# Performance work log

Measured on AMD Instinct MI355X. Metric: run time of the kernel, lower is better.

Reference implementation:

```python
import jax, jax.numpy as jnp
import numpy as np

NUM_BEAMS = 4
EOS = 2
PAD = 0
T = 16  # max_tokens decode steps
NEG = jnp.float32(-1e32)


def setup_inputs() -> dict:
    key = jax.random.key(0)
    ks = jax.random.split(key, 12)
    Vv, E, D, L, bs = 32000, 512, 512, 2, 16
    s = 0.05
    n = lambda k, sh: (jax.random.normal(k, sh, dtype=jnp.float32) * s)
    return {
        'inputs': jax.random.randint(ks[0], (1, bs), 0, Vv),
        'h0': n(ks[1], (L, bs, D)),
        'c0': n(ks[2], (L, bs, D)),
        'emb': n(ks[3], (Vv, E)),
        'Wih0': n(ks[4], (4 * D, E)),
        'Whh0': n(ks[5], (4 * D, D)),
        'b0': n(ks[6], (4 * D,)),
        'Wih1': n(ks[7], (4 * D, D)),
        'Whh1': n(ks[8], (4 * D, D)),
        'b1': n(ks[9], (4 * D,)),
        'Wp': n(ks[10], (D, Vv)),
        'bp': n(ks[11], (Vv,)),
    }


def _lstm(x, h, c, Wih, Whh, b):
    z = x @ Wih.T + h @ Whh.T + b
    i, f, g, o = jnp.split(z, 4, axis=-1)
    c = jax.nn.sigmoid(f) * c + jax.nn.sigmoid(i) * jnp.tanh(g)
    h = jax.nn.sigmoid(o) * jnp.tanh(c)
    return h, c


def reference(inputs, h0, c0, emb, Wih0, Whh0, b0, Wih1, Whh1, b1, Wp, bp):
    bs = inputs.shape[1]
    nb = NUM_BEAMS
    B = bs * nb
    Vv = emb.shape[0]

    def cell(tok, h, c):
        # one decode step of the 2-layer LSTM + projection; tok: (B,)
        x = emb[tok]
        h0n, c0n = _lstm(x, h[0], c[0], Wih0, Whh0, b0)
        h1n, c1n = _lstm(h0n, h[1], c[1], Wih1, Whh1, b1)
        logits = h1n @ Wp + bp  # (B, V)
        return logits, jnp.stack([h0n, h1n]), jnp.stack([c0n, c1n])

    offs = jnp.arange(bs)[:, None] * nb  # batch-major beam layout b*nb+beam

    # ---- iteration 0: all beams identical, keep beam 0 only ----
    tokens = jnp.repeat(inputs[0], nb)           # (B,)
    h = jnp.repeat(h0, nb, axis=1)               # (L, B, D)
    c = jnp.repeat(c0, nb, axis=1)
    logits0, h, c = cell(tokens, h, c)
    lp0 = jax.nn.log_softmax(logits0, axis=-1).reshape(bs, nb, Vv)[:, 0, :]
    logprobs, beams = jax.lax.top_k(lp0, nb)     # (bs, nb)
    pidx = (beams // Vv + offs).reshape(-1)      # parents == 0
    tokens = (beams % Vv).reshape(-1)
    h = h[:, pidx]
    c = c[:, pidx]
    finished = tokens == EOS
    beam_out = jnp.zeros((T + 1, B), dtype=tokens.dtype)
    beam_out = beam_out.at[0].set(jnp.repeat(inputs[0], nb)[pidx]).at[1].set(tokens)

    # ---- iterations 1..T-1 ----
    def step(carry, t):
        tokens, h, c, logprobs, finished, beam_out = carry
        logits, h, c = cell(tokens, h, c)
        new_lp = jax.nn.log_softmax(logits, axis=-1).reshape(bs, nb, Vv) + logprobs[:, :, None]
        # finished beams: forced to emit PAD with unchanged cumulative logprob
        masked = jnp.full((bs, nb, Vv), NEG).at[:, :, PAD].set(logprobs)
        fin = finished.reshape(bs, nb)
        new_lp = jnp.where(fin[:, :, None], masked, new_lp)
        logprobs, beams = jax.lax.top_k(new_lp.reshape(bs, nb * Vv), nb)
        pidx = (beams // Vv + offs).reshape(-1)
        toks = (beams % Vv).reshape(-1)
        h = h[:, pidx]
        c = c[:, pidx]
        finished = finished[pidx] | (toks == EOS)
        beam_out = beam_out[:, pidx].at[t + 1].set(toks)
        return (toks, h, c, logprobs, finished, beam_out), logits

    carry0 = (tokens, h, c, logprobs, finished, beam_out)
    carry_f, logits_seq = jax.lax.scan(step, carry0, jnp.arange(1, T))
    logits_all = jnp.concatenate([logits0[None], logits_seq], axis=0)  # (T, B, V)
    beam_outputs = carry_f[5].reshape(T + 1, bs, nb)
    return logits_all, beam_outputs
```

## Files before the change

### kernel.cpp

```cpp
#include <hip/hip_runtime.h>
#include <math.h>

#define BS     16
#define NB     4
#define BB     64
#define DD     512
#define VV     32000
#define TSTEPS 16
#define EOSTOK 2
#define NEGF   (-1e32f)
#define VT     64
#define NVT    (VV / VT)

__device__ __forceinline__ bool better(float av, int ai, float bv, int bi_) {
    return (av > bv) || (av == bv && ai < bi_);
}

__device__ __forceinline__ void glds4(const float* src, float* dst) {
    __builtin_amdgcn_global_load_lds((const __attribute__((address_space(1))) void*)src,
                                     (__attribute__((address_space(3))) void*)dst, 4, 0, 0);
}
__device__ __forceinline__ void glds16(const float* src, float* dst) {
    __builtin_amdgcn_global_load_lds((const __attribute__((address_space(1))) void*)src,
                                     (__attribute__((address_space(3))) void*)dst, 16, 0, 0);
}

__global__ void init_kernel(const int* __restrict__ inputs,
                            const float* __restrict__ h0, const float* __restrict__ c0,
                            float* __restrict__ h0s, float* __restrict__ c0s,
                            float* __restrict__ h1s, float* __restrict__ c1s,
                            int* __restrict__ tokens, int* __restrict__ pidx,
                            int* __restrict__ fin, float* __restrict__ lp,
                            int* __restrict__ bo)
{
    int tid = blockIdx.x * blockDim.x + threadIdx.x;
    int total = BB * DD;
    for (int i = tid; i < total; i += gridDim.x * blockDim.x) {
        int b = i / DD;
        int d = i % DD;
        int src0 = 0 * BS * DD + (b >> 2) * DD + d;
        int src1 = 1 * BS * DD + (b >> 2) * DD + d;
        h0s[i] = h0[src0];
        c0s[i] = c0[src0];
        h1s[i] = h0[src1];
        c1s[i] = c0[src1];
    }
    if (tid < BB) {
        tokens[tid] = inputs[tid >> 2];
        pidx[tid]   = tid;
        fin[tid]    = 0;
        lp[tid]     = 0.0f;
        bo[0 * BB + tid] = inputs[tid >> 2];
        for (int r = 1; r <= TSTEPS; r++) bo[r * BB + tid] = 0;
    }
}

__global__ __launch_bounds__(256) void lstm_kernel(
    const float* __restrict__ xbase, const int* __restrict__ xrow,
    const float* __restrict__ hsrc,  const float* __restrict__ csrc,
    const int* __restrict__ prow,
    float* __restrict__ hdst, float* __restrict__ cdst,
    const float* __restrict__ Wih, const float* __restrict__ Whh,
    const float* __restrict__ bias)
{
    __shared__ float U[64][129];
    __shared__ float Wl[4][1024];
    __shared__ double Z[4][64];
    __shared__ int rows_s[64], prows_s[64];
    int tid = threadIdx.x;
    int j = blockIdx.x;
    int b = tid & 63;
    int g = tid >> 6;
    int lane = tid & 63;
    int w = tid >> 6;

    #pragma unroll
    for (int i = 0; i < 4; i++) {
        int s0 = i * 256 + w * 64;
        int gg = s0 >> 8;
        int hh = (s0 >> 7) & 1;
        int c0 = s0 & 127;
        const float* rowbase = (hh ? Whh : Wih) + (size_t)(gg * DD + j) * DD;
        glds16(rowbase + 4 * (c0 + lane), (float*)Wl + 4 * s0);
    }
    if (tid < 64) {
        rows_s[tid]  = xrow ? xrow[tid] : tid;
        prows_s[tid] = prow[tid];
    }

    double a0 = 0.0, a1 = 0.0, a2 = 0.0, a3 = 0.0;
    for (int ch = 0; ch < 8; ch++) {
        int k0 = ch * 128;
        __syncthreads();
        #pragma unroll
        for (int i = 0; i < 32; i++) {
            int e0 = i * 256 + w * 64;
            int bb = e0 >> 7;
            int kk0 = e0 & 127;
            const float* src;
            if (k0 < 512) src = xbase + (size_t)rows_s[bb] * DD + k0 + kk0 + lane;
            else          src = hsrc + (size_t)prows_s[bb] * DD + (k0 - 512) + kk0 + lane;
            glds4(src, &U[bb][kk0]);
        }
        __syncthreads();
        const float* Wrow = &Wl[g][k0];
        #pragma unroll 8
        for (int kk = 0; kk < 128; kk += 4) {
            a0 = fma((double)U[b][kk + 0], (double)Wrow[kk + 0], a0);
            a1 = fma((double)U[b][kk + 1], (double)Wrow[kk + 1], a1);
            a2 = fma((double)U[b][kk + 2], (double)Wrow[kk + 2], a2);
            a3 = fma((double)U[b][kk + 3], (double)Wrow[kk + 3], a3);
        }
    }
    Z[g][b] = ((a0 + a1) + (a2 + a3));
    __syncthreads();

    if (tid < 64) {
        double zi = Z[0][b] + (double)bias[0 * DD + j];
        double zf = Z[1][b] + (double)bias[1 * DD + j];
        double zg = Z[2][b] + (double)bias[2 * DD + j];
        double zo = Z[3][b] + (double)bias[3 * DD + j];
        double si = 1.0 / (1.0 + exp(-zi));
        double sf = 1.0 / (1.0 + exp(-zf));
        double so = 1.0 / (1.0 + exp(-zo));
        double cold = (double)csrc[(size_t)prows_s[b] * DD + j];
        double cn = sf * cold + si * tanh(zg);
        double hn = so * tanh(cn);
        hdst[b * DD + j] = (float)hn;
        cdst[b * DD + j] = (float)cn;
    }
}

__global__ __launch_bounds__(256) void proj_kernel(
    const float* __restrict__ h1, const float* __restrict__ Wp,
    const float* __restrict__ bp, float* __restrict__ outf)
{
    __shared__ float sh[64][68];
    __shared__ float sw[64][68];
    int vbase = blockIdx.x * VT;
    int tid = threadIdx.x;
    int lane = tid & 63;
    int w = tid >> 6;
    int b0 = (tid >> 4) * 4;
    int v0 = (tid & 15) * 4;

    double acc[4][4];
    #pragma unroll
    for (int i = 0; i < 4; i++)
        #pragma unroll
        for (int q = 0; q < 4; q++) acc[i][q] = 0.0;

    for (int ch = 0; ch < 8; ch++) {
        int k0 = ch * 64;
        __syncthreads();
        #pragma unroll
        for (int i = 0; i < 16; i++) {
            int bb = i * 4 + w;
            glds4(h1 + (size_t)bb * DD + k0 + lane, &sh[bb][0]);
        }
        #pragma unroll
        for (int i = 0; i < 16; i++) {
            int kk = i * 4 + w;
            glds4(Wp + (size_t)(k0 + kk) * VV + vbase + lane, &sw[kk][0]);
        }
        __syncthreads();
        #pragma unroll
        for (int k4 = 0; k4 < 16; k4++) {
            int k = k4 * 4;
            float4 h4[4], w4[4];
            #pragma unroll
            for (int i = 0; i < 4; i++) h4[i] = *(const float4*)&sh[b0 + i][k];
            #pragma unroll
            for (int kk = 0; kk < 4; kk++) w4[kk] = *(const float4*)&sw[k + kk][v0];
            #pragma unroll
            for (int i = 0; i < 4; i++) {
                const float hh[4] = {h4[i].x, h4[i].y, h4[i].z, h4[i].w};
                #pragma unroll
                for (int kk = 0; kk < 4; kk++) {
                    double hd = (double)hh[kk];
                    const float ww[4] = {w4[kk].x, w4[kk].y, w4[kk].z, w4[kk].w};
                    #pragma unroll
                    for (int q = 0; q < 4; q++)
                        acc[i][q] = fma(hd, (double)ww[q], acc[i][q]);
                }
            }
        }
    }

    #pragma unroll
    for (int i = 0; i < 4; i++) {
        int brow = b0 + i;
        #pragma unroll
        for (int q = 0; q < 4; q++) {
            int v = vbase + v0 + q;
            outf[(size_t)brow * VV + v] = (float)(acc[i][q] + (double)bp[v]);
        }
    }
}

#define NPT 32
__global__ __launch_bounds__(1024) void row_kernel(
    const float* __restrict__ outf, const float* __restrict__ lp,
    const int* __restrict__ fin,
    float* __restrict__ rcv, int* __restrict__ rci, int step0)
{
    int row = blockIdx.x;
    int j   = row & 3;
    int tid = threadIdx.x;
    int base_idx = j * VV;

    float lp_r = step0 ? 0.0f : lp[row];
    int   f    = step0 ? 0    : fin[row];
    if (step0 && j != 0) {
        if (tid < 4) { rcv[row * 4 + tid] = NEGF; rci[row * 4 + tid] = base_idx + tid; }
        return;
    }
    if (f) {
        if (tid < 4) {
            rcv[row * 4 + tid] = (tid == 0) ? lp_r : NEGF;
            rci[row * 4 + tid] = base_idx + tid;
        }
        return;
    }

    const float* xo = outf + (size_t)row * VV;
    __shared__ double red[1024];

    float zreg[NPT];
    double m = -1e300;
    #pragma unroll
    for (int q = 0; q < NPT; q++) {
        int i = tid + q * 1024;
        float zf = 0.0f;
        if (i < VV) {
            zf = xo[i];
            m = fmax(m, (double)zf);
        }
        zreg[q] = zf;
    }

    red[tid] = m; __syncthreads();
    for (int s = 512; s > 0; s >>= 1) {
        if (tid < s) red[tid] = fmax(red[tid], red[tid + s]);
        __syncthreads();
    }
    m = red[0];
    __syncthreads();

    double sum = 0.0;
    #pragma unroll
    for (int q = 0; q < NPT; q++) {
        int i = tid + q * 1024;
        if (i < VV) sum += exp((double)zreg[q] - m);
    }
    red[tid] = sum; __syncthreads();
    for (int s = 512; s > 0; s >>= 1) {
        if (tid < s) red[tid] += red[tid + s];
        __syncthreads();
    }
    double lse = m + log(red[0]);
    __syncthreads();

    float bv[4]; int bx[4];
    #pragma unroll
    for (int q = 0; q < 4; q++) { bv[q] = -3.4e38f; bx[q] = 0x7fffffff; }
    #pragma unroll
    for (int q = 0; q < NPT; q++) {
        int i = tid + q * 1024;
        if (i < VV) {
            float lgp32 = (float)((double)zreg[q] - lse);
            float val   = (float)((double)lp_r + (double)lgp32);
            int idx = base_idx + i;
            if (better(val, idx, bv[3], bx[3])) {
                bv[3] = val; bx[3] = idx;
                #pragma unroll
                for (int s = 3; s > 0; s--) {
                    if (better(bv[s], bx[s], bv[s - 1], bx[s - 1])) {
                        float tv2 = bv[s]; bv[s] = bv[s - 1]; bv[s - 1] = tv2;
                        int ti2 = bx[s]; bx[s] = bx[s - 1]; bx[s - 1] = ti2;
                    }
                }
            }
        }
    }

    __shared__ float sv[1024][4];
    __shared__ int   si_[1024][4];
    #pragma unroll
    for (int q = 0; q < 4; q++) { sv[tid][q] = bv[q]; si_[tid][q] = bx[q]; }
    __syncthreads();
    for (int s = 512; s > 0; s >>= 1) {
        if (tid < s) {
            float av[4], ov[4], mv[4]; int ai[4], oi[4], mi[4];
            #pragma unroll
            for (int q = 0; q < 4; q++) {
                av[q] = sv[tid][q];     ai[q] = si_[tid][q];
                ov[q] = sv[tid + s][q]; oi[q] = si_[tid + s][q];
            }
            int pa = 0, pb = 0;
            #pragma unroll
            for (int q = 0; q < 4; q++) {
                bool takeA = (pb >= 4) || (pa < 4 && better(av[pa], ai[pa], ov[pb], oi[pb]));
                if (takeA) { mv[q] = av[pa]; mi[q] = ai[pa]; pa++; }
                else       { mv[q] = ov[pb]; mi[q] = oi[pb]; pb++; }
            }
            #pragma unroll
            for (int q = 0; q < 4; q++) { sv[tid][q] = mv[q]; si_[tid][q] = mi[q]; }
        }
        __syncthreads();
    }
    if (tid < 4) {
        rcv[row * 4 + tid] = sv[0][tid];
        rci[row * 4 + tid] = si_[0][tid];
    }
}

__global__ void merge_update_kernel(
    const float* __restrict__ rcv, const int* __restrict__ rci,
    float* __restrict__ lp, int* __restrict__ fin,
    int* __restrict__ tokens, int* __restrict__ pidx,
    int* __restrict__ bo, int t)
{
    int b = threadIdx.x;
    int bi = b >> 2, r = b & 3;

    float cv[16]; int ci[16];
    #pragma unroll
    for (int c = 0; c < 16; c++) { cv[c] = rcv[bi * 16 + c]; ci[c] = rci[bi * 16 + c]; }

    int sel = 0;
    #pragma unroll
    for (int c = 0; c < 16; c++) {
        int rank = 0;
        #pragma unroll
        for (int d = 0; d < 16; d++)
            if (d != c && better(cv[d], ci[d], cv[c], ci[c])) rank++;
        if (rank == r) sel = c;
    }

    float v = cv[sel];
    int flat = ci[sel];
    int q = flat / VV;
    int p = q + bi * 4;
    int tok = flat - q * VV;
    int oldfin = fin[p];
    int col[TSTEPS + 1];
    #pragma unroll
    for (int rr = 0; rr <= TSTEPS; rr++) col[rr] = bo[rr * BB + p];
    __syncthreads();
    #pragma unroll
    for (int rr = 0; rr <= TSTEPS; rr++) bo[rr * BB + b] = col[rr];
    bo[(t + 1) * BB + b] = tok;
    fin[b]    = oldfin | (tok == EOSTOK);
    lp[b]     = v;
    tokens[b] = tok;
    pidx[b]   = p;
}

__global__ void final_kernel(const int* __restrict__ bo, float* __restrict__ out)
{
    int i = blockIdx.x * blockDim.x + threadIdx.x;
    if (i < (TSTEPS + 1) * BB) out[i] = (float)bo[i];
}

extern "C" void kernel_launch(void* const* d_in, const int* in_sizes, int n_in,
                              void* d_out, int out_size, void* d_ws, size_t ws_size,
                              hipStream_t stream)
{
    const int*   inputs = (const int*)d_in[0];
    const float* h0   = (const float*)d_in[1];
    const float* c0   = (const float*)d_in[2];
    const float* emb  = (const float*)d_in[3];
    const float* Wih0 = (const float*)d_in[4];
    const float* Whh0 = (const float*)d_in[5];
    const float* b0   = (const float*)d_in[6];
    const float* Wih1 = (const float*)d_in[7];
    const float* Whh1 = (const float*)d_in[8];
    const float* b1   = (const float*)d_in[9];
    const float* Wp   = (const float*)d_in[10];
    const float* bp   = (const float*)d_in[11];
    float* out = (float*)d_out;

    char* w = (char*)d_ws;
    size_t off = 0;
    auto alloc = [&](size_t bytes) { void* p = w + off; off += (bytes + 255) & ~255ULL; return p; };
    float* h0s[2], *c0s[2], *h1s[2], *c1s[2];
    for (int s = 0; s < 2; s++) {
        h0s[s] = (float*)alloc(BB * DD * 4);
        c0s[s] = (float*)alloc(BB * DD * 4);
        h1s[s] = (float*)alloc(BB * DD * 4);
        c1s[s] = (float*)alloc(BB * DD * 4);
    }
    float* rcv   = (float*)alloc(BB * 4 * 4);
    int*   rci   = (int*)alloc(BB * 4 * 4);
    float* lp    = (float*)alloc(BB * 4);
    int* pidx    = (int*)alloc(BB * 4);
    int* tokens  = (int*)alloc(BB * 4);
    int* fin     = (int*)alloc(BB * 4);
    int* bo      = (int*)alloc((TSTEPS + 1) * BB * 4);

    init_kernel<<<128, 256, 0, stream>>>(inputs, h0, c0,
                                         h0s[0], c0s[0], h1s[0], c1s[0],
                                         tokens, pidx, fin, lp, bo);

    for (int t = 0; t < TSTEPS; t++) {
        int s = t & 1, d2 = s ^ 1;
        lstm_kernel<<<512, 256, 0, stream>>>(emb, tokens, h0s[s], c0s[s], pidx,
                                             h0s[d2], c0s[d2], Wih0, Whh0, b0);
        lstm_kernel<<<512, 256, 0, stream>>>(h0s[d2], nullptr, h1s[s], c1s[s], pidx,
                                             h1s[d2], c1s[d2], Wih1, Whh1, b1);

        float* outf = out + (size_t)t * BB * VV;
        proj_kernel<<<NVT, 256, 0, stream>>>(h1s[d2], Wp, bp, outf);
        row_kernel<<<BB, 1024, 0, stream>>>(outf, lp, fin, rcv, rci, t == 0 ? 1 : 0);
        merge_update_kernel<<<1, 64, 0, stream>>>(rcv, rci, lp, fin, tokens, pidx, bo, t);
    }
    final_kernel<<<5, 256, 0, stream>>>(bo, out + (size_t)TSTEPS * BB * VV);
}
```

Measured before the change: 2.851 ms.

## Double-buffer LDS staging in LSTM and projection kernels

New measurement: 2.916 ms. 1.02x slower.

```diff
diff --git a/kernel.cpp b/kernel.cpp
--- a/kernel.cpp
+++ b/kernel.cpp
@@ -63,7 +63,7 @@
     const float* __restrict__ Wih, const float* __restrict__ Whh,
     const float* __restrict__ bias)
 {
-    __shared__ float U[64][129];
+    __shared__ float U[2][64][65];
     __shared__ float Wl[4][1024];
     __shared__ double Z[4][64];
     __shared__ int rows_s[64], prows_s[64];
@@ -87,30 +87,36 @@
         rows_s[tid]  = xrow ? xrow[tid] : tid;
         prows_s[tid] = prow[tid];
     }
+    __syncthreads();
+
+    auto stage = [&](int ch, int buf) {
+        int k0 = ch * 64;
+        #pragma unroll
+        for (int i = 0; i < 16; i++) {
+            int bb = i * 4 + w;
+            const float* src;
+            if (k0 < 512) src = xbase + (size_t)rows_s[bb] * DD + k0 + lane;
+            else          src = hsrc + (size_t)prows_s[bb] * DD + (k0 - 512) + lane;
+            glds4(src, &U[buf][bb][0]);
+        }
+    };
+
+    stage(0, 0);
+    __syncthreads();
 
     double a0 = 0.0, a1 = 0.0, a2 = 0.0, a3 = 0.0;
-    for (int ch = 0; ch < 8; ch++) {
-        int k0 = ch * 128;
+    for (int ch = 0; ch < 16; ch++) {
+        int cur = ch & 1;
+        if (ch < 15) stage(ch + 1, cur ^ 1);
+        const float* Wrow = &Wl[g][ch * 64];
+        #pragma unroll 8
+        for (int kk = 0; kk < 64; kk += 4) {
+            a0 = fma((double)U[cur][b][kk + 0], (double)Wrow[kk + 0], a0);
+            a1 = fma((double)U[cur][b][kk + 1], (double)Wrow[kk + 1], a1);
+            a2 = fma((double)U[cur][b][kk + 2], (double)Wrow[kk + 2], a2);
+            a3 = fma((double)U[cur][b][kk + 3], (double)Wrow[kk + 3], a3);
+        }
         __syncthreads();
-        #pragma unroll
-        for (int i = 0; i < 32; i++) {
-            int e0 = i * 256 + w * 64;
-            int bb = e0 >> 7;
-            int kk0 = e0 & 127;
-            const float* src;
-            if (k0 < 512) src = xbase + (size_t)rows_s[bb] * DD + k0 + kk0 + lane;
-            else          src = hsrc + (size_t)prows_s[bb] * DD + (k0 - 512) + kk0 + lane;
-            glds4(src, &U[bb][kk0]);
-        }
-        __syncthreads();
-        const float* Wrow = &Wl[g][k0];
-        #pragma unroll 8
-        for (int kk = 0; kk < 128; kk += 4) {
-            a0 = fma((double)U[b][kk + 0], (double)Wrow[kk + 0], a0);
-            a1 = fma((double)U[b][kk + 1], (double)Wrow[kk + 1], a1);
-            a2 = fma((double)U[b][kk + 2], (double)Wrow[kk + 2], a2);
-            a3 = fma((double)U[b][kk + 3], (double)Wrow[kk + 3], a3);
-        }
     }
     Z[g][b] = ((a0 + a1) + (a2 + a3));
     __syncthreads();
@@ -135,8 +141,8 @@
     const float* __restrict__ h1, const float* __restrict__ Wp,
     const float* __restrict__ bp, float* __restrict__ outf)
 {
-    __shared__ float sh[64][68];
-    __shared__ float sw[64][68];
+    __shared__ float sh[2][64][68];
+    __shared__ float sw[2][64][68];
     int vbase = blockIdx.x * VT;
     int tid = threadIdx.x;
     int lane = tid & 63;
@@ -144,34 +150,40 @@
     int b0 = (tid >> 4) * 4;
     int v0 = (tid & 15) * 4;
 
-    double acc[4][4];
-    #pragma unroll
-    for (int i = 0; i < 4; i++)
-        #pragma unroll
-        for (int q = 0; q < 4; q++) acc[i][q] = 0.0;
-
-    for (int ch = 0; ch < 8; ch++) {
+    auto stage = [&](int ch, int buf) {
         int k0 = ch * 64;
-        __syncthreads();
         #pragma unroll
         for (int i = 0; i < 16; i++) {
             int bb = i * 4 + w;
-            glds4(h1 + (size_t)bb * DD + k0 + lane, &sh[bb][0]);
+            glds4(h1 + (size_t)bb * DD + k0 + lane, &sh[buf][bb][0]);
         }
         #pragma unroll
         for (int i = 0; i < 16; i++) {
             int kk = i * 4 + w;
-            glds4(Wp + (size_t)(k0 + kk) * VV + vbase + lane, &sw[kk][0]);
-        }
-        __syncthreads();
+            glds4(Wp + (size_t)(k0 + kk) * VV + vbase + lane, &sw[buf][kk][0]);
+        }
+    };
+
+    double acc[4][4];
+    #pragma unroll
+    for (int i = 0; i < 4; i++)
+        #pragma unroll
+        for (int q = 0; q < 4; q++) acc[i][q] = 0.0;
+
+    stage(0, 0);
+    __syncthreads();
+
+    for (int ch = 0; ch < 8; ch++) {
+        int cur = ch & 1;
+        if (ch < 7) stage(ch + 1, cur ^ 1);
         #pragma unroll
         for (int k4 = 0; k4 < 16; k4++) {
             int k = k4 * 4;
             float4 h4[4], w4[4];
             #pragma unroll
-            for (int i = 0; i < 4; i++) h4[i] = *(const float4*)&sh[b0 + i][k];
-            #pragma unroll
-            for (int kk = 0; kk < 4; kk++) w4[kk] = *(const float4*)&sw[k + kk][v0];
+            for (int i = 0; i < 4; i++) h4[i] = *(const float4*)&sh[cur][b0 + i][k];
+            #pragma unroll
+            for (int kk = 0; kk < 4; kk++) w4[kk] = *(const float4*)&sw[cur][k + kk][v0];
             #pragma unroll
             for (int i = 0; i < 4; i++) {
                 const float hh[4] = {h4[i].x, h4[i].y, h4[i].z, h4[i].w};
@@ -185,6 +197,7 @@
                 }
             }
         }
+        __syncthreads();
     }
 
     #pragma unroll
```

## Split LSTM and projection work across more, smaller blocks

Applied to the files above, without the earlier changes.

After: 2.855 ms. About the same (+0.1%).

```diff
diff --git a/kernel.cpp b/kernel.cpp
--- a/kernel.cpp
+++ b/kernel.cpp
@@ -9,8 +9,8 @@
 #define TSTEPS 16
 #define EOSTOK 2
 #define NEGF   (-1e32f)
-#define VT     64
-#define NVT    (VV / VT)
+#define VT2    32
+#define NVT2   (VV / VT2)
 
 __device__ __forceinline__ bool better(float av, int ai, float bv, int bi_) {
     return (av > bv) || (av == bv && ai < bi_);
@@ -55,7 +55,7 @@
     }
 }
 
-__global__ __launch_bounds__(256) void lstm_kernel(
+__global__ __launch_bounds__(128) void lstm_kernel(
     const float* __restrict__ xbase, const int* __restrict__ xrow,
     const float* __restrict__ hsrc,  const float* __restrict__ csrc,
     const int* __restrict__ prow,
@@ -63,29 +63,30 @@
     const float* __restrict__ Wih, const float* __restrict__ Whh,
     const float* __restrict__ bias)
 {
-    __shared__ float U[64][129];
+    __shared__ float U[32][129];
     __shared__ float Wl[4][1024];
-    __shared__ double Z[4][64];
-    __shared__ int rows_s[64], prows_s[64];
+    __shared__ double Z[4][32];
+    __shared__ int rows_s[32], prows_s[32];
     int tid = threadIdx.x;
-    int j = blockIdx.x;
-    int b = tid & 63;
-    int g = tid >> 6;
+    int j  = blockIdx.x >> 1;
+    int bo_ = (blockIdx.x & 1) * 32;
+    int b = tid & 31;
+    int g = tid >> 5;
     int lane = tid & 63;
     int w = tid >> 6;
 
     #pragma unroll
-    for (int i = 0; i < 4; i++) {
-        int s0 = i * 256 + w * 64;
+    for (int i = 0; i < 8; i++) {
+        int s0 = (i * 2 + w) * 64;
         int gg = s0 >> 8;
         int hh = (s0 >> 7) & 1;
         int c0 = s0 & 127;
         const float* rowbase = (hh ? Whh : Wih) + (size_t)(gg * DD + j) * DD;
         glds16(rowbase + 4 * (c0 + lane), (float*)Wl + 4 * s0);
     }
-    if (tid < 64) {
-        rows_s[tid]  = xrow ? xrow[tid] : tid;
-        prows_s[tid] = prow[tid];
+    if (tid < 32) {
+        rows_s[tid]  = xrow ? xrow[bo_ + tid] : (bo_ + tid);
+        prows_s[tid] = prow[bo_ + tid];
     }
 
     double a0 = 0.0, a1 = 0.0, a2 = 0.0, a3 = 0.0;
@@ -94,9 +95,9 @@
         __syncthreads();
         #pragma unroll
         for (int i = 0; i < 32; i++) {
-            int e0 = i * 256 + w * 64;
-            int bb = e0 >> 7;
-            int kk0 = e0 & 127;
+            int s = i * 2 + w;
+            int bb = s >> 1;
+            int kk0 = (s & 1) * 64;
             const float* src;
             if (k0 < 512) src = xbase + (size_t)rows_s[bb] * DD + k0 + kk0 + lane;
             else          src = hsrc + (size_t)prows_s[bb] * DD + (k0 - 512) + kk0 + lane;
@@ -115,7 +116,8 @@
     Z[g][b] = ((a0 + a1) + (a2 + a3));
     __syncthreads();
 
-    if (tid < 64) {
+    if (tid < 32) {
+        int gb = bo_ + b;
         double zi = Z[0][b] + (double)bias[0 * DD + j];
         double zf = Z[1][b] + (double)bias[1 * DD + j];
         double zg = Z[2][b] + (double)bias[2 * DD + j];
@@ -126,8 +128,8 @@
         double cold = (double)csrc[(size_t)prows_s[b] * DD + j];
         double cn = sf * cold + si * tanh(zg);
         double hn = so * tanh(cn);
-        hdst[b * DD + j] = (float)hn;
-        cdst[b * DD + j] = (float)cn;
+        hdst[gb * DD + j] = (float)hn;
+        cdst[gb * DD + j] = (float)cn;
     }
 }
 
@@ -136,19 +138,17 @@
     const float* __restrict__ bp, float* __restrict__ outf)
 {
     __shared__ float sh[64][68];
-    __shared__ float sw[64][68];
-    int vbase = blockIdx.x * VT;
+    __shared__ float sw[64][32];
+    int vbase = blockIdx.x * VT2;
     int tid = threadIdx.x;
     int lane = tid & 63;
     int w = tid >> 6;
     int b0 = (tid >> 4) * 4;
-    int v0 = (tid & 15) * 4;
-
-    double acc[4][4];
-    #pragma unroll
-    for (int i = 0; i < 4; i++)
-        #pragma unroll
-        for (int q = 0; q < 4; q++) acc[i][q] = 0.0;
+    int v0 = (tid & 15) * 2;
+
+    double acc[4][2];
+    #pragma unroll
+    for (int i = 0; i < 4; i++) { acc[i][0] = 0.0; acc[i][1] = 0.0; }
 
     for (int ch = 0; ch < 8; ch++) {
         int k0 = ch * 64;
@@ -159,29 +159,29 @@
             glds4(h1 + (size_t)bb * DD + k0 + lane, &sh[bb][0]);
         }
         #pragma unroll
-        for (int i = 0; i < 16; i++) {
-            int kk = i * 4 + w;
-            glds4(Wp + (size_t)(k0 + kk) * VV + vbase + lane, &sw[kk][0]);
+        for (int i = 0; i < 8; i++) {
+            int r2 = i * 4 + w;
+            const float* src = Wp + (size_t)(k0 + 2 * r2 + (lane >> 5)) * VV
+                                  + vbase + (lane & 31);
+            glds4(src, &sw[2 * r2][0]);
         }
         __syncthreads();
         #pragma unroll
         for (int k4 = 0; k4 < 16; k4++) {
             int k = k4 * 4;
-            float4 h4[4], w4[4];
+            float4 h4[4]; float2 w2[4];
             #pragma unroll
             for (int i = 0; i < 4; i++) h4[i] = *(const float4*)&sh[b0 + i][k];
             #pragma unroll
-            for (int kk = 0; kk < 4; kk++) w4[kk] = *(const float4*)&sw[k + kk][v0];
+            for (int kk = 0; kk < 4; kk++) w2[kk] = *(const float2*)&sw[k + kk][v0];
             #pragma unroll
             for (int i = 0; i < 4; i++) {
                 const float hh[4] = {h4[i].x, h4[i].y, h4[i].z, h4[i].w};
                 #pragma unroll
                 for (int kk = 0; kk < 4; kk++) {
                     double hd = (double)hh[kk];
-                    const float ww[4] = {w4[kk].x, w4[kk].y, w4[kk].z, w4[kk].w};
-                    #pragma unroll
-                    for (int q = 0; q < 4; q++)
-                        acc[i][q] = fma(hd, (double)ww[q], acc[i][q]);
+                    acc[i][0] = fma(hd, (double)w2[kk].x, acc[i][0]);
+                    acc[i][1] = fma(hd, (double)w2[kk].y, acc[i][1]);
                 }
             }
         }
@@ -191,7 +191,7 @@
     for (int i = 0; i < 4; i++) {
         int brow = b0 + i;
         #pragma unroll
-        for (int q = 0; q < 4; q++) {
+        for (int q = 0; q < 2; q++) {
             int v = vbase + v0 + q;
             outf[(size_t)brow * VV + v] = (float)(acc[i][q] + (double)bp[v]);
         }
@@ -405,13 +405,13 @@
 
     for (int t = 0; t < TSTEPS; t++) {
         int s = t & 1, d2 = s ^ 1;
-        lstm_kernel<<<512, 256, 0, stream>>>(emb, tokens, h0s[s], c0s[s], pidx,
-                                             h0s[d2], c0s[d2], Wih0, Whh0, b0);
-        lstm_kernel<<<512, 256, 0, stream>>>(h0s[d2], nullptr, h1s[s], c1s[s], pidx,
-                                             h1s[d2], c1s[d2], Wih1, Whh1, b1);
+        lstm_kernel<<<1024, 128, 0, stream>>>(emb, tokens, h0s[s], c0s[s], pidx,
+                                              h0s[d2], c0s[d2], Wih0, Whh0, b0);
+        lstm_kernel<<<1024, 128, 0, stream>>>(h0s[d2], nullptr, h1s[s], c1s[s], pidx,
+                                              h1s[d2], c1s[d2], Wih1, Whh1, b1);
 
         float* outf = out + (size_t)t * BB * VV;
-        proj_kernel<<<NVT, 256, 0, stream>>>(h1s[d2], Wp, bp, outf);
+        proj_kernel<<<NVT2, 256, 0, stream>>>(h1s[d2], Wp, bp, outf);
         row_kernel<<<BB, 1024, 0, stream>>>(outf, lp, fin, rcv, rci, t == 0 ? 1 : 0);
         merge_update_kernel<<<1, 64, 0, stream>>>(rcv, rci, lp, fin, tokens, pidx, bo, t);
     }
```
